# Optimization experiments

Hardware: AMD Instinct MI355X
Metric: run time of the kernel (lower is better)

## Reference

```python
import jax, jax.numpy as jnp
from jax import lax
import numpy as np

M_FILTERS = 128   # rows of responses D
N_CHANNELS = 1024 # cols of responses D (spectral channels)
BATCH = 4096
N_LAYERS = 17
IMAX = 50


def setup_inputs() -> dict:
    key = jax.random.key(0)
    k1, k2, k3, k4 = jax.random.split(key, 4)
    t1 = jax.random.normal(k1, (BATCH, N_CHANNELS), dtype=jnp.float32)
    t2 = jax.random.normal(k2, (BATCH, N_CHANNELS), dtype=jnp.float32)
    params = jax.random.uniform(k3, (M_FILTERS, N_LAYERS), dtype=jnp.float32)
    responses = jax.random.normal(k4, (M_FILTERS, N_CHANNELS), dtype=jnp.float32)
    return {
        "t1": t1,
        "t2": t2,
        "params": params,
        "thick_min": jnp.float32(0.0),
        "thick_max": jnp.float32(1.0),
        "beta_range": jnp.float32(0.1),
        "responses": responses,
    }


def _coherence_reduce(D0):
    """Faithful vectorized version of the 50-iteration coherence-reduction loop.

    The original per-row Python loop (Ri[i] > Rth branch) only reads row i and
    pre-computed Rth/delta, so it is exactly a masked row update.
    torch.linalg.eig on the symmetric matrices G is replaced by eigh (same
    eigenpairs up to sign/order; order is fixed by the explicit descending sort,
    and only the top-M eigenpairs reach the output D[:M,:]).
    """
    Mr, Nr = D0.shape
    ratio = jnp.float32(Nr / Mr)
    eye_b = jnp.eye(Nr, dtype=bool)

    def body(_, D):
        D = D / jnp.linalg.norm(D)                      # Frobenius norm over (0,1)
        G = D.T @ D                                     # [N, N]
        Sigma, V = jnp.linalg.eigh(G)
        Sigma = jnp.where(jnp.abs(Sigma) > 1e-10, ratio, Sigma)
        G = (V * Sigma[None, :]) @ V.T                  # V diag(Sigma) V^T
        G0 = jnp.abs(G - jnp.diag(jnp.diag(G)))
        Ri = jnp.sum(G0, axis=0)                        # [N]
        Rth = jnp.min(Ri)
        delta = Rth / (Nr - 1)
        mask = (Ri > Rth)[:, None]                      # rows to clip
        Gn = jnp.where(mask, delta * jnp.sign(G), G)
        Gn = jnp.where(eye_b, G, Gn)                    # keep original diagonal
        G = (Gn + Gn.T) * 0.5
        Sigma, V = jnp.linalg.eigh(G)
        order = jnp.argsort(-Sigma)                     # descending
        Sigma = Sigma[order]
        V = V[:, order]
        # Original: Sigma[M:-1]=0 then D = diag(Sigma)^{1/2} @ V.T, D = D[:M,:].
        # Only the top-M eigenpairs contribute to the first M rows.
        Dn = jnp.power(Sigma[:Mr], 0.5)[:, None] * V[:, :Mr].T  # [M, N]
        return Dn

    return lax.fori_loop(0, IMAX, body, D0)


def reference(t1, t2, params, thick_min, thick_max, beta_range, responses):
    # HybnetLoss: MSE match loss + hinge range loss (filter_loss is zeroed in source)
    match_loss = jnp.mean((t1 - t2) ** 2)
    d = jnp.float32(0.01)
    res = jnp.maximum((params - thick_min - d) / (-d),
                      (params - thick_max + d) / d)
    range_loss = jnp.mean(jnp.maximum(res, jnp.zeros_like(res)))
    original_loss = match_loss + beta_range * range_loss

    # HybnetLoss_plus: coherence-reduction regularizer on the response matrix
    D = _coherence_reduce(responses)
    rloss = jnp.mean((D - responses) ** 2)
    return original_loss + rloss
```

## Files before the change

### kernel.cpp

```cpp
#include <hip/hip_runtime.h>

#define NBLK 256
#define NTHR 512

#define OFF_G    0
#define OFF_QT   1048576
#define OFF_Y    1179648
#define OFF_C    1703936
#define OFF_RP   1851392
#define OFF_ACC  1867776
#define OFF_BAR  1867792

#define CNT_A 0
#define CNT_B 1
#define CNT_C 2
#define CNT_E 3
#define FLG_A 8
#define FLG_B 9
#define FLG_C 10
#define FLG_E 11

typedef float v4f __attribute__((ext_vector_type(4)));

__device__ __forceinline__ void cld4_8(v4f& a, v4f& b, v4f& c, v4f& d,
                                       v4f& e, v4f& f, v4f& g, v4f& h,
                                       const float* pa, const float* pb,
                                       const float* pc, const float* pd,
                                       const float* pe, const float* pf,
                                       const float* pg, const float* ph) {
    asm volatile("global_load_dwordx4 %0, %8, off sc1\n\t"
                 "global_load_dwordx4 %1, %9, off sc1\n\t"
                 "global_load_dwordx4 %2, %10, off sc1\n\t"
                 "global_load_dwordx4 %3, %11, off sc1\n\t"
                 "global_load_dwordx4 %4, %12, off sc1\n\t"
                 "global_load_dwordx4 %5, %13, off sc1\n\t"
                 "global_load_dwordx4 %6, %14, off sc1\n\t"
                 "global_load_dwordx4 %7, %15, off sc1\n\t"
                 "s_waitcnt vmcnt(0)"
                 : "=&v"(a), "=&v"(b), "=&v"(c), "=&v"(d),
                   "=&v"(e), "=&v"(f), "=&v"(g), "=&v"(h)
                 : "v"(pa), "v"(pb), "v"(pc), "v"(pd),
                   "v"(pe), "v"(pf), "v"(pg), "v"(ph) : "memory");
}
__device__ __forceinline__ void cld4_4(v4f& a, v4f& b, v4f& c, v4f& d,
                                       const float* pa, const float* pb,
                                       const float* pc, const float* pd) {
    asm volatile("global_load_dwordx4 %0, %4, off sc1\n\t"
                 "global_load_dwordx4 %1, %5, off sc1\n\t"
                 "global_load_dwordx4 %2, %6, off sc1\n\t"
                 "global_load_dwordx4 %3, %7, off sc1\n\t"
                 "s_waitcnt vmcnt(0)"
                 : "=&v"(a), "=&v"(b), "=&v"(c), "=&v"(d)
                 : "v"(pa), "v"(pb), "v"(pc), "v"(pd) : "memory");
}
__device__ __forceinline__ void cld4_2(v4f& a, v4f& b,
                                       const float* pa, const float* pb) {
    asm volatile("global_load_dwordx4 %0, %2, off sc1\n\t"
                 "global_load_dwordx4 %1, %3, off sc1\n\t"
                 "s_waitcnt vmcnt(0)"
                 : "=&v"(a), "=&v"(b) : "v"(pa), "v"(pb) : "memory");
}
__device__ __forceinline__ void cld1_4(float& a, float& b, float& c, float& d,
                                       const float* pa, const float* pb,
                                       const float* pc, const float* pd) {
    asm volatile("global_load_dword %0, %4, off sc1\n\t"
                 "global_load_dword %1, %5, off sc1\n\t"
                 "global_load_dword %2, %6, off sc1\n\t"
                 "global_load_dword %3, %7, off sc1\n\t"
                 "s_waitcnt vmcnt(0)"
                 : "=&v"(a), "=&v"(b), "=&v"(c), "=&v"(d)
                 : "v"(pa), "v"(pb), "v"(pc), "v"(pd) : "memory");
}
__device__ __forceinline__ void cld1_8(float& a, float& b, float& c, float& d,
                                       float& e, float& f, float& g, float& h,
                                       const float* pa, const float* pb,
                                       const float* pc, const float* pd,
                                       const float* pe, const float* pf,
                                       const float* pg, const float* ph) {
    asm volatile("global_load_dword %0, %8, off sc1\n\t"
                 "global_load_dword %1, %9, off sc1\n\t"
                 "global_load_dword %2, %10, off sc1\n\t"
                 "global_load_dword %3, %11, off sc1\n\t"
                 "global_load_dword %4, %12, off sc1\n\t"
                 "global_load_dword %5, %13, off sc1\n\t"
                 "global_load_dword %6, %14, off sc1\n\t"
                 "global_load_dword %7, %15, off sc1\n\t"
                 "s_waitcnt vmcnt(0)"
                 : "=&v"(a), "=&v"(b), "=&v"(c), "=&v"(d),
                   "=&v"(e), "=&v"(f), "=&v"(g), "=&v"(h)
                 : "v"(pa), "v"(pb), "v"(pc), "v"(pd),
                   "v"(pe), "v"(pf), "v"(pg), "v"(ph) : "memory");
}
__device__ __forceinline__ void iss2(v4f& a, v4f& b,
                                     const float* pa, const float* pb) {
    asm volatile("global_load_dwordx4 %0, %2, off sc1\n\t"
                 "global_load_dwordx4 %1, %3, off sc1"
                 : "=&v"(a), "=&v"(b) : "v"(pa), "v"(pb) : "memory");
}
__device__ __forceinline__ void wt2(v4f& a, v4f& b) {
    asm volatile("s_waitcnt vmcnt(0)"
                 : "+v"(a), "+v"(b) :: "memory");
}
__device__ __forceinline__ void iss1(v4f& a, const float* pa) {
    asm volatile("global_load_dwordx4 %0, %1, off sc1"
                 : "=&v"(a) : "v"(pa) : "memory");
}
__device__ __forceinline__ void wt1(v4f& a) {
    asm volatile("s_waitcnt vmcnt(0)" : "+v"(a) :: "memory");
}

__device__ __forceinline__ void syncL() {
    asm volatile("s_waitcnt lgkmcnt(0)" ::: "memory");
    __builtin_amdgcn_s_barrier();
    asm volatile("" ::: "memory");
}

__device__ __forceinline__ void ast2(float* p, float a, float b) {
    union { unsigned long long u; float f[2]; } c; c.f[0] = a; c.f[1] = b;
    __hip_atomic_store((unsigned long long*)p, c.u,
                       __ATOMIC_RELAXED, __HIP_MEMORY_SCOPE_AGENT);
}
__device__ __forceinline__ float ald(const float* p) {
    return __hip_atomic_load(p, __ATOMIC_RELAXED, __HIP_MEMORY_SCOPE_AGENT);
}
__device__ __forceinline__ void ast(float* p, float x) {
    __hip_atomic_store(p, x, __ATOMIC_RELAXED, __HIP_MEMORY_SCOPE_AGENT);
}

__device__ __forceinline__ void bar_arrive(unsigned* bb, int cnt_line, int flg_line,
                                           unsigned trigger, unsigned flagval) {
    __syncthreads();
    if (threadIdx.x == 0) {
        unsigned old = __hip_atomic_fetch_add(bb + cnt_line * 16, 1u,
                                              __ATOMIC_RELAXED, __HIP_MEMORY_SCOPE_AGENT);
        if (old == trigger - 1u)
            __hip_atomic_fetch_max(bb + flg_line * 16, flagval,
                                   __ATOMIC_RELEASE, __HIP_MEMORY_SCOPE_AGENT);
    }
}
__device__ __forceinline__ void bar_wait(unsigned* bb, int flg_line, unsigned flagval) {
    if (threadIdx.x == 0) {
        while (__hip_atomic_load(bb + flg_line * 16,
                                 __ATOMIC_RELAXED, __HIP_MEMORY_SCOPE_AGENT) < flagval)
            __builtin_amdgcn_s_sleep(2);
    }
    __builtin_amdgcn_s_waitcnt(0);
    __syncthreads();
}

union Smem {
    struct { float As[32][68]; float Bs[32][68]; float Rs[64][17]; } gg;
    struct { float Cs[128][129]; float inv_d[16]; float irs[128];
             float Xs[16][64]; } chol;
    struct { float Ri[1024]; float red[512]; float As[32][36]; float Bs[32][68]; } gy;
    struct { float As[32][68]; float Bs[32][68]; float red[512]; } tb;
    float red[512];
};

__device__ __forceinline__ void dev_match(Smem* sm, const float* t1, const float* t2,
                                          float* accb, int w) {
    int tid = threadIdx.x;
    const float4* a = (const float4*)t1;
    const float4* b = (const float4*)t2;
    float s = 0.f;
    for (int i = w * 512 + tid; i < 1048576; i += 218 * 512) {
        float4 x = a[i], y = b[i];
        float d0 = x.x - y.x, d1 = x.y - y.y, d2 = x.z - y.z, d3 = x.w - y.w;
        s += d0 * d0 + d1 * d1 + d2 * d2 + d3 * d3;
    }
    sm->red[tid] = s; __syncthreads();
    for (int w2 = 256; w2 > 0; w2 >>= 1) {
        if (tid < w2) sm->red[tid] += sm->red[tid + w2];
        __syncthreads();
    }
    if (tid == 0) atomicAdd(&accb[0], sm->red[0]);
    __syncthreads();
}

__device__ __forceinline__ void dev_range(Smem* sm, const float* params, const float* tmin,
                                          const float* tmax, float* accb) {
    int tid = threadIdx.x;
    float a = tmin[0], b = tmax[0];
    const float d = 0.01f;
    float s = 0.f;
    for (int i = tid; i < 128 * 17; i += 512) {
        float p = params[i];
        float r1 = (p - a - d) / (-d);
        float r2 = (p - b + d) / d;
        s += fmaxf(fmaxf(r1, r2), 0.f);
    }
    sm->red[tid] = s; __syncthreads();
    for (int w = 256; w > 0; w >>= 1) {
        if (tid < w) sm->red[tid] += sm->red[tid + w];
        __syncthreads();
    }
    if (tid == 0) atomicAdd(&accb[1], sm->red[0]);
    __syncthreads();
}

__device__ __forceinline__ void dev_sumsq(Smem* sm, const float* X, float* accb, int w) {
    int tid = threadIdx.x;
    float s = 0.f;
    for (int i = w * 512 + tid; i < 131072; i += 2048) { float v = X[i]; s += v * v; }
    sm->red[tid] = s; __syncthreads();
    for (int w2 = 256; w2 > 0; w2 >>= 1) {
        if (tid < w2) sm->red[tid] += sm->red[tid + w2];
        __syncthreads();
    }
    if (tid == 0) atomicAdd(&accb[3], sm->red[0]);
    __syncthreads();
}

__device__ __forceinline__ void dev_syrk(Smem* sm, const float* A, const float* B,
                                         float* C, int bid) {
    int tid = threadIdx.x;
    int q0 = (bid & 1) * 64, p0 = ((bid >> 1) & 1) * 64, z = bid >> 2;
    int kc0 = z * 32;
    int p = tid & 63, kg = (tid >> 6) * 4;
    int tx = tid & 15, ty = tid >> 4;
    float acc[2][4] = {};
    v4f av, bv;
    cld4_2(av, bv, &A[(p0 + p) * 1024 + kc0 + kg], &B[(q0 + p) * 1024 + kc0 + kg]);
    sm->gg.As[kg + 0][p] = av.x; sm->gg.As[kg + 1][p] = av.y;
    sm->gg.As[kg + 2][p] = av.z; sm->gg.As[kg + 3][p] = av.w;
    sm->gg.Bs[kg + 0][p] = bv.x; sm->gg.Bs[kg + 1][p] = bv.y;
    sm->gg.Bs[kg + 2][p] = bv.z; sm->gg.Bs[kg + 3][p] = bv.w;
    __syncthreads();
    for (int k = 0; k < 32; ++k) {
        float2 a2 = *(const float2*)&sm->gg.As[k][ty * 2];
        float4 b4 = *(const float4*)&sm->gg.Bs[k][tx * 4];
        acc[0][0] += a2.x * b4.x; acc[0][1] += a2.x * b4.y;
        acc[0][2] += a2.x * b4.z; acc[0][3] += a2.x * b4.w;
        acc[1][0] += a2.y * b4.x; acc[1][1] += a2.y * b4.y;
        acc[1][2] += a2.y * b4.z; acc[1][3] += a2.y * b4.w;
    }
    #pragma unroll
    for (int i = 0; i < 2; ++i)
        #pragma unroll
        for (int j = 0; j < 4; ++j)
            atomicAdd(&C[(p0 + ty * 2 + i) * 128 + q0 + tx * 4 + j], acc[i][j]);
}

__device__ __forceinline__ void dev_cholTrsm(Smem* sm, const float* C, const float* RHS,
                                             float* Qt, int bid) {
    int tid = threadIdx.x;
    {
        const float* base = C + tid * 32;
        v4f z0, z1, z2, z3, z4, z5, z6, z7;
        cld4_8(z0, z1, z2, z3, z4, z5, z6, z7,
               base, base + 4, base + 8, base + 12,
               base + 16, base + 20, base + 24, base + 28);
        int r = tid >> 2, c0 = (tid & 3) * 32;
        *(v4f*)&sm->chol.Cs[r][c0]      = z0; *(v4f*)&sm->chol.Cs[r][c0 + 4]  = z1;
        *(v4f*)&sm->chol.Cs[r][c0 + 8]  = z2; *(v4f*)&sm->chol.Cs[r][c0 + 12] = z3;
        *(v4f*)&sm->chol.Cs[r][c0 + 16] = z4; *(v4f*)&sm->chol.Cs[r][c0 + 20] = z5;
        *(v4f*)&sm->chol.Cs[r][c0 + 24] = z6; *(v4f*)&sm->chol.Cs[r][c0 + 28] = z7;
    }
    __syncthreads();
    int lane = tid & 63;
    for (int kb = 0; kb < 8; ++kb) {
        int k0 = kb * 16;
        if (tid < 64) {
            float P0[16], P1[16], invs[16];
            #pragma unroll
            for (int u = 0; u < 16; ++u) {
                P0[u] = sm->chol.Cs[lane][k0 + u];
                P1[u] = sm->chol.Cs[lane + 64][k0 + u];
            }
            #pragma unroll
            for (int kk = 0; kk < 16; ++kk) {
                int k = k0 + kk;
                int src = k & 63;
                bool hi = (k >= 64);
                float pr[16];
                #pragma unroll
                for (int u = 0; u < 16; ++u)
                    if (u >= kk) pr[u] = __shfl(hi ? P1[u] : P0[u], src);
                float inv = __builtin_amdgcn_rcpf(pr[kk]);
                invs[kk] = inv;
                float f0 = (lane > k) ? P0[kk] * inv : 0.f;
                float f1 = ((lane + 64) > k) ? P1[kk] * inv : 0.f;
                #pragma unroll
                for (int u = kk + 1; u < 16; ++u) {
                    P0[u] -= f0 * pr[u];
                    P1[u] -= f1 * pr[u];
                }
            }
            #pragma unroll
            for (int u = 0; u < 16; ++u) {
                sm->chol.Cs[lane][k0 + u] = P0[u];
                sm->chol.Cs[lane + 64][k0 + u] = P1[u];
            }
            if (lane == 0) {
                #pragma unroll
                for (int kk = 0; kk < 16; ++kk) sm->chol.inv_d[kk] = invs[kk];
            }
        }
        __syncthreads();
        int base = k0 + 16;
        if (base < 128) {
            int hh = tid >> 6, cc = tid & 63;
            int j1 = base + cc;
            int j2 = base + cc + 64;
            bool has1 = (j1 < 128), has2 = (j2 < 128);
            float w1[16], w2[16];
            if (has1) {
                #pragma unroll
                for (int u = 0; u < 16; ++u) w1[u] = sm->chol.Cs[j1][k0 + u] * sm->chol.inv_d[u];
            }
            if (has2) {
                #pragma unroll
                for (int u = 0; u < 16; ++u) w2[u] = sm->chol.Cs[j2][k0 + u] * sm->chol.inv_d[u];
            }
            int rlo = hh * 16;
            int istart = rlo > base ? rlo : base;
            for (int i = istart; i < rlo + 16; ++i) {
                float v[16];
                #pragma unroll
                for (int u = 0; u < 16; ++u) v[u] = sm->chol.Cs[i][k0 + u];
                float a1 = 0.f, a2 = 0.f;
                #pragma unroll
                for (int u = 0; u < 16; ++u) { a1 += v[u] * w1[u]; a2 += v[u] * w2[u]; }
                if (has1) sm->chol.Cs[i][j1] -= a1;
                if (has2) sm->chol.Cs[i][j2] -= a2;
            }
        }
        __syncthreads();
    }
    if (tid < 128) sm->chol.irs[tid] = __builtin_amdgcn_rsqf(sm->chol.Cs[tid][tid]);
    int c = tid & 63, h = tid >> 6;
    int j0 = bid * 64;
    float acc[16];
    {
        const float* p = &RHS[(h * 16) * 1024 + j0 + c];
        cld1_8(acc[0], acc[1], acc[2], acc[3], acc[4], acc[5], acc[6], acc[7],
               p, p + 1024, p + 2048, p + 3072, p + 4096, p + 5120, p + 6144, p + 7168);
        cld1_8(acc[8], acc[9], acc[10], acc[11], acc[12], acc[13], acc[14], acc[15],
               p + 8192, p + 9216, p + 10240, p + 11264,
               p + 12288, p + 13312, p + 14336, p + 15360);
    }
    __syncthreads();
    for (int pb = 0; pb < 8; ++pb) {
        int p0 = pb * 16;
        if (h == pb) {
            #pragma unroll
            for (int kk = 0; kk < 16; ++kk) {
                int k = p0 + kk;
                float irsk = sm->chol.irs[k];
                float x = acc[kk] * irsk;
                acc[kk] = x;
                sm->chol.Xs[kk][c] = x;
                float xs = x * irsk;
                #pragma unroll
                for (int r = kk + 1; r < 16; ++r)
                    acc[r] -= sm->chol.Cs[p0 + r][k] * xs;
            }
        }
        __syncthreads();
        if (h > pb) {
            int rb = h * 16;
            #pragma unroll
            for (int kk = 0; kk < 16; ++kk) {
                int k = p0 + kk;
                float xs = sm->chol.Xs[kk][c] * sm->chol.irs[k];
                #pragma unroll
                for (int r = 0; r < 16; ++r)
                    acc[r] -= sm->chol.Cs[rb + r][k] * xs;
            }
        }
        __syncthreads();
    }
    #pragma unroll
    for (int r = 0; r < 16; ++r)
        ast(&Qt[(h * 16 + r) * 1024 + j0 + c], acc[r]);
}

__device__ __forceinline__ void dev_gemmG(Smem* sm, const float* Qt, float* G,
                                          float* Rpart, int bid) {
    int tid = threadIdx.x;
    int tx = tid & 15, ty = tid >> 4;
    int bx = bid & 15, by = bid >> 4;
    int a0 = by * 64, b0 = bx * 64;
    int r0 = tid >> 4, c4 = (tid & 15) << 2;
    float acc[2][4] = {};
    v4f av, bv;
    iss2(av, bv, &Qt[r0 * 1024 + a0 + c4], &Qt[r0 * 1024 + b0 + c4]);
    for (int kc = 0; kc < 128; kc += 32) {
        wt2(av, bv);
        *(v4f*)&sm->gg.As[r0][c4] = av;
        *(v4f*)&sm->gg.Bs[r0][c4] = bv;
        syncL();
        if (kc < 96) {
            int kn = kc + 32;
            iss2(av, bv, &Qt[(kn + r0) * 1024 + a0 + c4],
                 &Qt[(kn + r0) * 1024 + b0 + c4]);
        }
        for (int k = 0; k < 32; ++k) {
            float2 a2 = *(const float2*)&sm->gg.As[k][ty * 2];
            float4 b4 = *(const float4*)&sm->gg.Bs[k][tx * 4];
            acc[0][0] += a2.x * b4.x; acc[0][1] += a2.x * b4.y;
            acc[0][2] += a2.x * b4.z; acc[0][3] += a2.x * b4.w;
            acc[1][0] += a2.y * b4.x; acc[1][1] += a2.y * b4.y;
            acc[1][2] += a2.y * b4.z; acc[1][3] += a2.y * b4.w;
        }
        syncL();
    }
    float rsum[2] = {0.f, 0.f};
    #pragma unroll
    for (int i = 0; i < 2; ++i) {
        int aa = a0 + ty * 2 + i;
        float g[4];
        #pragma unroll
        for (int j = 0; j < 4; ++j) g[j] = 8.f * acc[i][j];
        float* gp = &G[aa * 1024 + b0 + tx * 4];
        ast2(gp, g[0], g[1]);
        ast2(gp + 2, g[2], g[3]);
        int bb = b0 + tx * 4;
        #pragma unroll
        for (int j = 0; j < 4; ++j) rsum[i] += (aa == bb + j) ? 0.f : fabsf(g[j]);
    }
    sm->gg.Rs[ty * 2 + 0][tx] = rsum[0];
    sm->gg.Rs[ty * 2 + 1][tx] = rsum[1];
    __syncthreads();
    if (tid < 64) {
        float s = 0.f;
        #pragma unroll
        for (int x = 0; x < 16; ++x) s += sm->gg.Rs[tid][x];
        ast(&Rpart[(a0 + tid) * 16 + bx], s);
    }
}

__device__ __forceinline__ void dev_ri(Smem* sm, const float* Rpart,
                                       float* rth, float* delta) {
    int tid = threadIdx.x;
    int e0 = tid, e1 = tid + 512;
    v4f t0, t1, t2, t3, u0, u1, u2, u3;
    cld4_8(t0, t1, t2, t3, u0, u1, u2, u3,
           &Rpart[e0 * 16], &Rpart[e0 * 16 + 4],
           &Rpart[e0 * 16 + 8], &Rpart[e0 * 16 + 12],
           &Rpart[e1 * 16], &Rpart[e1 * 16 + 4],
           &Rpart[e1 * 16 + 8], &Rpart[e1 * 16 + 12]);
    float s0 = 0.f;
    s0 += t0.x; s0 += t0.y; s0 += t0.z; s0 += t0.w;
    s0 += t1.x; s0 += t1.y; s0 += t1.z; s0 += t1.w;
    s0 += t2.x; s0 += t2.y; s0 += t2.z; s0 += t2.w;
    s0 += t3.x; s0 += t3.y; s0 += t3.z; s0 += t3.w;
    float s1 = 0.f;
    s1 += u0.x; s1 += u0.y; s1 += u0.z; s1 += u0.w;
    s1 += u1.x; s1 += u1.y; s1 += u1.z; s1 += u1.w;
    s1 += u2.x; s1 += u2.y; s1 += u2.z; s1 += u2.w;
    s1 += u3.x; s1 += u3.y; s1 += u3.z; s1 += u3.w;
    sm->gy.Ri[e0] = s0;
    sm->gy.Ri[e1] = s1;
    float mn = fminf(s0, s1);
    #pragma unroll
    for (int off = 32; off > 0; off >>= 1)
        mn = fminf(mn, __shfl_xor(mn, off));
    if ((tid & 63) == 0) sm->gy.red[tid >> 6] = mn;
    __syncthreads();
    float r = sm->gy.red[0];
    #pragma unroll
    for (int w = 1; w < 8; ++w) r = fminf(r, sm->gy.red[w]);
    *rth = r;
    *delta = r / 1023.f;
}

__device__ __forceinline__ void dev_gemmY(Smem* sm, const float* Qt, const float* G,
                                          float rth, float delta, float* Y, int bid) {
    int tid = threadIdx.x;
    int j0 = (bid & 15) * 64;
    int m0 = ((bid >> 4) & 3) * 32;
    int kz = bid >> 6;
    int kc0 = kz * 256;
    int tx = tid & 15, ty = tid >> 4;
    int m = (tid & 255) >> 3, k4 = (tid & 7) << 2;
    int rg = tid >> 4, cg = (tid & 15) << 2;
    float acc[4] = {};
    v4f q, g0;
    if (tid < 256) iss1(q, &Qt[(m0 + m) * 1024 + kc0 + k4]);
    iss1(g0, &G[(kc0 + rg) * 1024 + j0 + cg]);
    for (int kc = kc0; kc < kc0 + 256; kc += 32) {
        wt1(g0);
        if (tid < 256) {
            wt1(q);
            *(v4f*)&sm->gy.As[m][k4] = q;
        }
        {
            int a = kc + rg;
            float ria = sm->gy.Ri[a];
            v4f bw;
            #pragma unroll
            for (int u = 0; u < 4; ++u) {
                int b = j0 + cg + u;
                float g = g0[u];
                float sg = delta * ((g > 0.f) ? 1.f : ((g < 0.f) ? -1.f : 0.f));
                float ga = (ria > rth) ? sg : g;
                float gb = (sm->gy.Ri[b] > rth) ? sg : g;
                bw[u] = (a == b) ? g : 0.5f * (ga + gb);
            }
            *(v4f*)&sm->gy.Bs[rg][cg] = bw;
        }
        syncL();
        if (kc < kc0 + 224) {
            int kn = kc + 32;
            if (tid < 256) iss1(q, &Qt[(m0 + m) * 1024 + kn + k4]);
            iss1(g0, &G[(kn + rg) * 1024 + j0 + cg]);
        }
        #pragma unroll
        for (int kb = 0; kb < 8; ++kb) {
            v4f qa = *(const v4f*)&sm->gy.As[ty][kb * 4];
            #pragma unroll
            for (int kk = 0; kk < 4; ++kk) {
                float4 b4 = *(const float4*)&sm->gy.Bs[kb * 4 + kk][tx * 4];
                float a = qa[kk];
                acc[0] += a * b4.x; acc[1] += a * b4.y;
                acc[2] += a * b4.z; acc[3] += a * b4.w;
            }
        }
        syncL();
    }
    #pragma unroll
    for (int j = 0; j < 4; ++j)
        atomicAdd(&Y[(m0 + ty) * 1024 + j0 + tx * 4 + j], acc[j]);
}

__device__ __forceinline__ void dev_trB(Smem* sm, const float* Qt, const float* G,
                                        const float* Rpart, float* accb, int bid) {
    int tid = threadIdx.x;
    float rth, delta;
    dev_ri(sm, Rpart, &rth, &delta);
    __syncthreads();
    int tx = tid & 15, ty = tid >> 4;
    int a0 = (bid >> 4) * 64, b0 = (bid & 15) * 64;
    int r0 = tid >> 4, c4 = (tid & 15) << 2;
    float acc[2][4] = {};
    for (int kc = 0; kc < 128; kc += 32) {
        v4f av, bv;
        cld4_2(av, bv, &Qt[(kc + r0) * 1024 + a0 + c4],
               &Qt[(kc + r0) * 1024 + b0 + c4]);
        *(v4f*)&sm->tb.As[r0][c4] = av;
        *(v4f*)&sm->tb.Bs[r0][c4] = bv;
        __syncthreads();
        for (int k = 0; k < 32; ++k) {
            float2 a2 = *(const float2*)&sm->tb.As[k][ty * 2];
            float4 b4 = *(const float4*)&sm->tb.Bs[k][tx * 4];
            acc[0][0] += a2.x * b4.x; acc[0][1] += a2.x * b4.y;
            acc[0][2] += a2.x * b4.z; acc[0][3] += a2.x * b4.w;
            acc[1][0] += a2.y * b4.x; acc[1][1] += a2.y * b4.y;
            acc[1][2] += a2.y * b4.z; acc[1][3] += a2.y * b4.w;
        }
        __syncthreads();
    }
    float rib[4];
    #pragma unroll
    for (int j = 0; j < 4; ++j) {
        int bb = b0 + tx * 4 + j;
        v4f t0, t1, t2, t3;
        cld4_4(t0, t1, t2, t3, &Rpart[bb * 16], &Rpart[bb * 16 + 4],
               &Rpart[bb * 16 + 8], &Rpart[bb * 16 + 12]);
        float s = 0.f;
        s += t0.x; s += t0.y; s += t0.z; s += t0.w;
        s += t1.x; s += t1.y; s += t1.z; s += t1.w;
        s += t2.x; s += t2.y; s += t2.z; s += t2.w;
        s += t3.x; s += t3.y; s += t3.z; s += t3.w;
        rib[j] = s;
    }
    float s = 0.f;
    #pragma unroll
    for (int i = 0; i < 2; ++i) {
        int aa = a0 + ty * 2 + i;
        v4f t0, t1, t2, t3;
        cld4_4(t0, t1, t2, t3, &Rpart[aa * 16], &Rpart[aa * 16 + 4],
               &Rpart[aa * 16 + 8], &Rpart[aa * 16 + 12]);
        float ria = 0.f;
        ria += t0.x; ria += t0.y; ria += t0.z; ria += t0.w;
        ria += t1.x; ria += t1.y; ria += t1.z; ria += t1.w;
        ria += t2.x; ria += t2.y; ria += t2.z; ria += t2.w;
        ria += t3.x; ria += t3.y; ria += t3.z; ria += t3.w;
        float g0, g1, g2, g3;
        const float* gp = &G[aa * 1024 + b0 + tx * 4];
        cld1_4(g0, g1, g2, g3, gp, gp + 1, gp + 2, gp + 3);
        float gv[4] = {g0, g1, g2, g3};
        #pragma unroll
        for (int j = 0; j < 4; ++j) {
            int bb = b0 + tx * 4 + j;
            float g = gv[j];
            float sg = delta * ((g > 0.f) ? 1.f : ((g < 0.f) ? -1.f : 0.f));
            float ga = (ria > rth) ? sg : g;
            float gb = (rib[j] > rth) ? sg : g;
            float gp2 = (aa == bb) ? g : 0.5f * (ga + gb);
            s += gp2 * acc[i][j];
        }
    }
    __syncthreads();
    sm->tb.red[tid] = s;
    __syncthreads();
    for (int w = 256; w > 0; w >>= 1) {
        if (tid < w) sm->tb.red[tid] += sm->tb.red[tid + w];
        __syncthreads();
    }
    if (tid == 0) atomicAdd(&accb[2], sm->tb.red[0]);
}

__global__ __launch_bounds__(512) void mega(const float* __restrict__ t1,
                                            const float* __restrict__ t2,
                                            const float* __restrict__ params,
                                            const float* __restrict__ tmin,
                                            const float* __restrict__ tmax,
                                            const float* __restrict__ beta,
                                            const float* __restrict__ R,
                                            float* ws, float* out) {
    float* G     = ws + OFF_G;
    float* Qt    = ws + OFF_QT;
    float* Y     = ws + OFF_Y;
    float* C     = ws + OFF_C;
    float* Rpart = ws + OFF_RP;
    float* accb  = ws + OFF_ACC;
    unsigned* bb = (unsigned*)(ws + OFF_BAR);
    __shared__ Smem sm;
    int bid = blockIdx.x;
    int tid = threadIdx.x;
    unsigned phA = 0, phB = 0, phC = 0, phE = 0, trgC = 0;

    if (bid < 32) {
        ast(&C[bid * 512 + tid], 0.f);
    } else if (bid < 250) dev_match(&sm, t1, t2, accb, bid - 32);
    else if (bid == 250) dev_range(&sm, params, tmin, tmax, accb);
    else if (bid < 255) dev_sumsq(&sm, R, accb, bid - 251);
    trgC += 32; ++phC;
    if (bid < 32) bar_arrive(bb, CNT_C, FLG_C, trgC, phC);
    trgC += 128; ++phC;
    if (bid < 128) {
        bar_wait(bb, FLG_C, phC - 1);
        dev_syrk(&sm, R, R, C, bid);
        bar_arrive(bb, CNT_C, FLG_C, trgC, phC);
    }
    ++phE;
    if (bid < 16) {
        bar_wait(bb, FLG_C, phC);
        dev_cholTrsm(&sm, C, R, Qt, bid);
        bar_arrive(bb, CNT_E, FLG_E, phE * 16, phE);
    }
    bar_wait(bb, FLG_E, phE);

    for (int it = 0; it < 50; ++it) {
        dev_gemmG(&sm, Qt, G, Rpart, bid);
        ast(&Y[bid * 512 + tid], 0.f);
        if (bid < 32) ast(&C[bid * 512 + tid], 0.f);
        ++phA;
        bar_arrive(bb, CNT_A, FLG_A, phA * 256, phA);
        bar_wait(bb, FLG_A, phA);
        {
            float rth, delta;
            dev_ri(&sm, Rpart, &rth, &delta);
            dev_gemmY(&sm, Qt, G, rth, delta, Y, bid);
        }
        ++phB;
        bar_arrive(bb, CNT_B, FLG_B, phB * 256, phB);
        trgC += 128; ++phC;
        if (bid < 128) {
            bar_wait(bb, FLG_B, phB);
            dev_syrk(&sm, Y, Y, C, bid);
            bar_arrive(bb, CNT_C, FLG_C, trgC, phC);
        }
        ++phE;
        if (bid < 16) {
            bar_wait(bb, FLG_C, phC);
            dev_cholTrsm(&sm, C, Y, Qt, bid);
            bar_arrive(bb, CNT_E, FLG_E, phE * 16, phE);
        }
        bar_wait(bb, FLG_E, phE);
    }

    dev_trB(&sm, Qt, G, Rpart, accb, bid);
    ++phA;
    bar_arrive(bb, CNT_A, FLG_A, phA * 256, phA);
    if (bid == 0) {
        bar_wait(bb, FLG_A, phA);
        if (tid == 0)
            out[0] = ald(&accb[0]) / 4194304.f + beta[0] * (ald(&accb[1]) / 2176.f)
                   + (ald(&accb[2]) + ald(&accb[3])) / 131072.f;
    }
}

extern "C" void kernel_launch(void* const* d_in, const int* in_sizes, int n_in,
                              void* d_out, int out_size, void* d_ws, size_t ws_size,
                              hipStream_t stream) {
    const float* t1 = (const float*)d_in[0];
    const float* t2 = (const float*)d_in[1];
    const float* params = (const float*)d_in[2];
    const float* tmin = (const float*)d_in[3];
    const float* tmax = (const float*)d_in[4];
    const float* beta = (const float*)d_in[5];
    const float* R = (const float*)d_in[6];
    float* ws = (float*)d_ws;
    float* out = (float*)d_out;

    hipMemsetAsync(ws + OFF_ACC, 0, 9280, stream);
    mega<<<NBLK, NTHR, 0, stream>>>(t1, t2, params, tmin, tmax, beta, R, ws, out);
}
```

Measured before the change: 7.256 ms.

## Fuse Gram SYRK into Cholesky blocks, removing a grid barrier per iteration

Drops the separate distributed SYRK stage, which used 128 blocks with atomics into C and its own barrier. Each of the 16 Cholesky/TRSM blocks now recomputes the full 128x128 Gram matrix redundantly in LDS from Y. Y is stored transposed so these loads are contiguous. This removes one grid-wide barrier and the C zeroing/atomics per iteration, at the cost of 16x redundant GEMM work (128x128x1024 per block) on the critical path.

Measured after the change: 20.16 ms. 178% more time.

```diff
diff --git a/kernel.cpp b/kernel.cpp
--- a/kernel.cpp
+++ b/kernel.cpp
@@ -5,19 +5,16 @@
 
 #define OFF_G    0
 #define OFF_QT   1048576
-#define OFF_Y    1179648
-#define OFF_C    1703936
+#define OFF_YT   1179648
 #define OFF_RP   1851392
 #define OFF_ACC  1867776
 #define OFF_BAR  1867792
 
 #define CNT_A 0
 #define CNT_B 1
-#define CNT_C 2
 #define CNT_E 3
 #define FLG_A 8
 #define FLG_B 9
-#define FLG_C 10
 #define FLG_E 11
 
 typedef float v4f __attribute__((ext_vector_type(4)));
@@ -150,8 +147,8 @@
 
 union Smem {
     struct { float As[32][68]; float Bs[32][68]; float Rs[64][17]; } gg;
-    struct { float Cs[128][129]; float inv_d[16]; float irs[128];
-             float Xs[16][64]; } chol;
+    struct { float Cs[128][129]; float Yts[32][129]; float inv_d[16];
+             float irs[128]; float Xs[16][64]; } chol;
     struct { float Ri[1024]; float red[512]; float As[32][36]; float Bs[32][68]; } gy;
     struct { float As[32][68]; float Bs[32][68]; float red[512]; } tb;
     float red[512];
@@ -211,51 +208,55 @@
     __syncthreads();
 }
 
-__device__ __forceinline__ void dev_syrk(Smem* sm, const float* A, const float* B,
-                                         float* C, int bid) {
-    int tid = threadIdx.x;
-    int q0 = (bid & 1) * 64, p0 = ((bid >> 1) & 1) * 64, z = bid >> 2;
-    int kc0 = z * 32;
-    int p = tid & 63, kg = (tid >> 6) * 4;
-    int tx = tid & 15, ty = tid >> 4;
-    float acc[2][4] = {};
-    v4f av, bv;
-    cld4_2(av, bv, &A[(p0 + p) * 1024 + kc0 + kg], &B[(q0 + p) * 1024 + kc0 + kg]);
-    sm->gg.As[kg + 0][p] = av.x; sm->gg.As[kg + 1][p] = av.y;
-    sm->gg.As[kg + 2][p] = av.z; sm->gg.As[kg + 3][p] = av.w;
-    sm->gg.Bs[kg + 0][p] = bv.x; sm->gg.Bs[kg + 1][p] = bv.y;
-    sm->gg.Bs[kg + 2][p] = bv.z; sm->gg.Bs[kg + 3][p] = bv.w;
-    __syncthreads();
-    for (int k = 0; k < 32; ++k) {
-        float2 a2 = *(const float2*)&sm->gg.As[k][ty * 2];
-        float4 b4 = *(const float4*)&sm->gg.Bs[k][tx * 4];
-        acc[0][0] += a2.x * b4.x; acc[0][1] += a2.x * b4.y;
-        acc[0][2] += a2.x * b4.z; acc[0][3] += a2.x * b4.w;
-        acc[1][0] += a2.y * b4.x; acc[1][1] += a2.y * b4.y;
-        acc[1][2] += a2.y * b4.z; acc[1][3] += a2.y * b4.w;
-    }
-    #pragma unroll
-    for (int i = 0; i < 2; ++i)
-        #pragma unroll
-        for (int j = 0; j < 4; ++j)
-            atomicAdd(&C[(p0 + ty * 2 + i) * 128 + q0 + tx * 4 + j], acc[i][j]);
-}
-
-__device__ __forceinline__ void dev_cholTrsm(Smem* sm, const float* C, const float* RHS,
-                                             float* Qt, int bid) {
-    int tid = threadIdx.x;
-    {
-        const float* base = C + tid * 32;
-        v4f z0, z1, z2, z3, z4, z5, z6, z7;
-        cld4_8(z0, z1, z2, z3, z4, z5, z6, z7,
-               base, base + 4, base + 8, base + 12,
-               base + 16, base + 20, base + 24, base + 28);
-        int r = tid >> 2, c0 = (tid & 3) * 32;
-        *(v4f*)&sm->chol.Cs[r][c0]      = z0; *(v4f*)&sm->chol.Cs[r][c0 + 4]  = z1;
-        *(v4f*)&sm->chol.Cs[r][c0 + 8]  = z2; *(v4f*)&sm->chol.Cs[r][c0 + 12] = z3;
-        *(v4f*)&sm->chol.Cs[r][c0 + 16] = z4; *(v4f*)&sm->chol.Cs[r][c0 + 20] = z5;
-        *(v4f*)&sm->chol.Cs[r][c0 + 24] = z6; *(v4f*)&sm->chol.Cs[r][c0 + 28] = z7;
-    }
+__device__ __forceinline__ void dev_cholFused(Smem* sm, const float* SRC,
+                                              const float* RHS, float* Qt,
+                                              int bid, int srcT, int rhsT) {
+    int tid = threadIdx.x;
+    int I = tid >> 4, J = tid & 15;
+    float acc[4][8];
+    #pragma unroll
+    for (int i = 0; i < 4; ++i)
+        #pragma unroll
+        for (int j = 0; j < 8; ++j) acc[i][j] = 0.f;
+    for (int kc = 0; kc < 1024; kc += 32) {
+        if (srcT) {
+            int k = tid >> 4, c8 = (tid & 15) * 8;
+            v4f u0, u1;
+            const float* p = &SRC[(kc + k) * 128 + c8];
+            cld4_2(u0, u1, p, p + 4);
+            *(v4f*)&sm->chol.Yts[k][c8] = u0;
+            *(v4f*)&sm->chol.Yts[k][c8 + 4] = u1;
+        } else {
+            int r = tid >> 2, kq = (tid & 3) * 8;
+            v4f u0, u1;
+            const float* p = &SRC[r * 1024 + kc + kq];
+            cld4_2(u0, u1, p, p + 4);
+            #pragma unroll
+            for (int j = 0; j < 4; ++j) sm->chol.Yts[kq + j][r] = u0[j];
+            #pragma unroll
+            for (int j = 0; j < 4; ++j) sm->chol.Yts[kq + 4 + j][r] = u1[j];
+        }
+        __syncthreads();
+        for (int k = 0; k < 32; ++k) {
+            v4f a = *(const v4f*)&sm->chol.Yts[k][I * 4];
+            v4f b0 = *(const v4f*)&sm->chol.Yts[k][J * 8];
+            v4f b1 = *(const v4f*)&sm->chol.Yts[k][J * 8 + 4];
+            #pragma unroll
+            for (int i = 0; i < 4; ++i) {
+                #pragma unroll
+                for (int j = 0; j < 4; ++j) {
+                    acc[i][j]     += a[i] * b0[j];
+                    acc[i][j + 4] += a[i] * b1[j];
+                }
+            }
+        }
+        __syncthreads();
+    }
+    #pragma unroll
+    for (int i = 0; i < 4; ++i)
+        #pragma unroll
+        for (int j = 0; j < 8; ++j)
+            sm->chol.Cs[I * 4 + i][J * 8 + j] = acc[i][j];
     __syncthreads();
     int lane = tid & 63;
     for (int kb = 0; kb < 8; ++kb) {
@@ -330,12 +331,21 @@
     if (tid < 128) sm->chol.irs[tid] = __builtin_amdgcn_rsqf(sm->chol.Cs[tid][tid]);
     int c = tid & 63, h = tid >> 6;
     int j0 = bid * 64;
-    float acc[16];
-    {
+    float acc2[16];
+    if (rhsT) {
+        const float* p = &RHS[(j0 + c) * 128 + h * 16];
+        v4f t0, t1, t2, t3;
+        cld4_4(t0, t1, t2, t3, p, p + 4, p + 8, p + 12);
+        #pragma unroll
+        for (int u = 0; u < 4; ++u) {
+            acc2[u] = t0[u]; acc2[4 + u] = t1[u];
+            acc2[8 + u] = t2[u]; acc2[12 + u] = t3[u];
+        }
+    } else {
         const float* p = &RHS[(h * 16) * 1024 + j0 + c];
-        cld1_8(acc[0], acc[1], acc[2], acc[3], acc[4], acc[5], acc[6], acc[7],
+        cld1_8(acc2[0], acc2[1], acc2[2], acc2[3], acc2[4], acc2[5], acc2[6], acc2[7],
                p, p + 1024, p + 2048, p + 3072, p + 4096, p + 5120, p + 6144, p + 7168);
-        cld1_8(acc[8], acc[9], acc[10], acc[11], acc[12], acc[13], acc[14], acc[15],
+        cld1_8(acc2[8], acc2[9], acc2[10], acc2[11], acc2[12], acc2[13], acc2[14], acc2[15],
                p + 8192, p + 9216, p + 10240, p + 11264,
                p + 12288, p + 13312, p + 14336, p + 15360);
     }
@@ -347,13 +357,13 @@
             for (int kk = 0; kk < 16; ++kk) {
                 int k = p0 + kk;
                 float irsk = sm->chol.irs[k];
-                float x = acc[kk] * irsk;
-                acc[kk] = x;
+                float x = acc2[kk] * irsk;
+                acc2[kk] = x;
                 sm->chol.Xs[kk][c] = x;
                 float xs = x * irsk;
                 #pragma unroll
                 for (int r = kk + 1; r < 16; ++r)
-                    acc[r] -= sm->chol.Cs[p0 + r][k] * xs;
+                    acc2[r] -= sm->chol.Cs[p0 + r][k] * xs;
             }
         }
         __syncthreads();
@@ -365,14 +375,14 @@
                 float xs = sm->chol.Xs[kk][c] * sm->chol.irs[k];
                 #pragma unroll
                 for (int r = 0; r < 16; ++r)
-                    acc[r] -= sm->chol.Cs[rb + r][k] * xs;
+                    acc2[r] -= sm->chol.Cs[rb + r][k] * xs;
             }
         }
         __syncthreads();
     }
     #pragma unroll
     for (int r = 0; r < 16; ++r)
-        ast(&Qt[(h * 16 + r) * 1024 + j0 + c], acc[r]);
+        ast(&Qt[(h * 16 + r) * 1024 + j0 + c], acc2[r]);
 }
 
 __device__ __forceinline__ void dev_gemmG(Smem* sm, const float* Qt, float* G,
@@ -466,7 +476,7 @@
 }
 
 __device__ __forceinline__ void dev_gemmY(Smem* sm, const float* Qt, const float* G,
-                                          float rth, float delta, float* Y, int bid) {
+                                          float rth, float delta, float* Yt, int bid) {
     int tid = threadIdx.x;
     int j0 = (bid & 15) * 64;
     int m0 = ((bid >> 4) & 3) * 32;
@@ -521,7 +531,7 @@
     }
     #pragma unroll
     for (int j = 0; j < 4; ++j)
-        atomicAdd(&Y[(m0 + ty) * 1024 + j0 + tx * 4 + j], acc[j]);
+        atomicAdd(&Yt[(j0 + tx * 4 + j) * 128 + m0 + ty], acc[j]);
 }
 
 __device__ __forceinline__ void dev_trB(Smem* sm, const float* Qt, const float* G,
@@ -612,61 +622,43 @@
                                             float* ws, float* out) {
     float* G     = ws + OFF_G;
     float* Qt    = ws + OFF_QT;
-    float* Y     = ws + OFF_Y;
-    float* C     = ws + OFF_C;
+    float* Yt    = ws + OFF_YT;
     float* Rpart = ws + OFF_RP;
     float* accb  = ws + OFF_ACC;
     unsigned* bb = (unsigned*)(ws + OFF_BAR);
     __shared__ Smem sm;
     int bid = blockIdx.x;
     int tid = threadIdx.x;
-    unsigned phA = 0, phB = 0, phC = 0, phE = 0, trgC = 0;
-
-    if (bid < 32) {
-        ast(&C[bid * 512 + tid], 0.f);
-    } else if (bid < 250) dev_match(&sm, t1, t2, accb, bid - 32);
-    else if (bid == 250) dev_range(&sm, params, tmin, tmax, accb);
-    else if (bid < 255) dev_sumsq(&sm, R, accb, bid - 251);
-    trgC += 32; ++phC;
-    if (bid < 32) bar_arrive(bb, CNT_C, FLG_C, trgC, phC);
-    trgC += 128; ++phC;
-    if (bid < 128) {
-        bar_wait(bb, FLG_C, phC - 1);
-        dev_syrk(&sm, R, R, C, bid);
-        bar_arrive(bb, CNT_C, FLG_C, trgC, phC);
+    unsigned phA = 0, phB = 0, phE = 0;
+
+    if (bid >= 16) {
+        if (bid < 234) dev_match(&sm, t1, t2, accb, bid - 16);
+        else if (bid == 234) dev_range(&sm, params, tmin, tmax, accb);
+        else if (bid < 239) dev_sumsq(&sm, R, accb, bid - 235);
+    } else {
+        dev_cholFused(&sm, R, R, Qt, bid, 0, 0);
     }
     ++phE;
-    if (bid < 16) {
-        bar_wait(bb, FLG_C, phC);
-        dev_cholTrsm(&sm, C, R, Qt, bid);
-        bar_arrive(bb, CNT_E, FLG_E, phE * 16, phE);
-    }
+    if (bid < 16) bar_arrive(bb, CNT_E, FLG_E, phE * 16, phE);
     bar_wait(bb, FLG_E, phE);
 
     for (int it = 0; it < 50; ++it) {
         dev_gemmG(&sm, Qt, G, Rpart, bid);
-        ast(&Y[bid * 512 + tid], 0.f);
-        if (bid < 32) ast(&C[bid * 512 + tid], 0.f);
+        ast(&Yt[bid * 512 + tid], 0.f);
         ++phA;
         bar_arrive(bb, CNT_A, FLG_A, phA * 256, phA);
         bar_wait(bb, FLG_A, phA);
         {
             float rth, delta;
             dev_ri(&sm, Rpart, &rth, &delta);
-            dev_gemmY(&sm, Qt, G, rth, delta, Y, bid);
+            dev_gemmY(&sm, Qt, G, rth, delta, Yt, bid);
         }
         ++phB;
         bar_arrive(bb, CNT_B, FLG_B, phB * 256, phB);
-        trgC += 128; ++phC;
-        if (bid < 128) {
-            bar_wait(bb, FLG_B, phB);
-            dev_syrk(&sm, Y, Y, C, bid);
-            bar_arrive(bb, CNT_C, FLG_C, trgC, phC);
-        }
         ++phE;
         if (bid < 16) {
-            bar_wait(bb, FLG_C, phC);
-            dev_cholTrsm(&sm, C, Y, Qt, bid);
+            bar_wait(bb, FLG_B, phB);
+            dev_cholFused(&sm, Yt, Yt, Qt, bid, 1, 1);
             bar_arrive(bb, CNT_E, FLG_E, phE * 16, phE);
         }
         bar_wait(bb, FLG_E, phE);
```
